# Kernel optimization log

Measured on AMD Instinct MI355X. Metric: run time of the kernel, lower is better.

The kernel has to match this reference:

```python
import jax, jax.numpy as jnp
import numpy as np

N_NODES = 50000
N_EDGES = 800000
N_GRAPHS = 64
F_IN = 256
F_HID = 256
F_OUT = 128


def setup_inputs() -> dict:
    key = jax.random.key(0)
    ks = jax.random.split(key, 8)
    x = jax.random.normal(ks[0], (N_NODES, F_IN), jnp.float32)
    edge_index = jax.random.randint(ks[1], (2, N_EDGES), 0, N_NODES, jnp.int32)
    batch = jnp.sort(jax.random.randint(ks[2], (N_NODES,), 0, N_GRAPHS, jnp.int32))
    W1 = jax.random.normal(ks[3], (F_IN, F_HID), jnp.float32) / np.sqrt(F_IN)
    b1 = jnp.zeros((F_HID,), jnp.float32)
    W2 = jax.random.normal(ks[4], (F_HID, F_HID), jnp.float32) / np.sqrt(F_HID)
    b2 = jnp.zeros((F_HID,), jnp.float32)
    Wfc = jax.random.normal(ks[5], (3 * F_HID, F_OUT), jnp.float32) / np.sqrt(3 * F_HID)
    bfc = jnp.zeros((F_OUT,), jnp.float32)
    return {"x": x, "edge_index": edge_index, "batch": batch, "n_graphs": N_GRAPHS,
            "W1": W1, "b1": b1, "W2": W2, "b2": b2, "Wfc": Wfc, "bfc": bfc}


def _gcn_layer(h, src, dst, norm, W, b, n_nodes):
    # transform first (F_in -> F_out), then gather-normalize-scatter
    h = h @ W                                      # [N, F]
    msg = h[src] * norm[:, None]                   # [E+N, F]
    agg = jax.ops.segment_sum(msg, dst, num_segments=n_nodes)
    return agg + b


def reference(x, edge_index, batch, n_graphs, W1, b1, W2, b2, Wfc, bfc):
    n = x.shape[0]
    # eval mode: dropout_adj / F.dropout are identity
    loops = jnp.arange(n, dtype=edge_index.dtype)
    src = jnp.concatenate([edge_index[0], loops])  # A + I
    dst = jnp.concatenate([edge_index[1], loops])
    # symmetric normalization D^-1/2 (A+I) D^-1/2 (degree counted at dst)
    deg = jax.ops.segment_sum(jnp.ones_like(dst, jnp.float32), dst, num_segments=n)
    dinv = jax.lax.rsqrt(jnp.maximum(deg, 1.0))    # deg >= 1 (self loops)
    norm = dinv[src] * dinv[dst]

    h = jax.nn.relu(_gcn_layer(x, src, dst, norm, W1, b1, n))
    h = jax.nn.relu(_gcn_layer(h, src, dst, norm, W2, b2, n))

    # triple global pooling over graph ids
    sums = jax.ops.segment_sum(h, batch, num_segments=n_graphs)           # add pool
    cnts = jax.ops.segment_sum(jnp.ones((n,), h.dtype), batch, num_segments=n_graphs)
    mean = sums / jnp.maximum(cnts, 1.0)[:, None]                          # mean pool
    mx = jax.ops.segment_max(h, batch, num_segments=n_graphs)             # max pool
    mx = jnp.where(jnp.isfinite(mx), mx, 0.0)                              # empty-segment guard

    g = jnp.concatenate([mean, mx, sums], axis=1)  # [G, 3*F_HID]
    return g @ Wfc + bfc
```

## Files before the change

kernel.cpp:

```cpp
#include <hip/hip_runtime.h>

#define N_NODES 50000
#define N_EDGES 800000
#define N_GRAPHS 64
#define F 256
#define F_OUT 128
#define G_DIM 768
#define SCAN_NB ((N_NODES + 255) / 256)
#define POOL_CHUNKS 32

typedef unsigned short ushort_t;
typedef short short8 __attribute__((ext_vector_type(8)));
typedef unsigned short ushort8 __attribute__((ext_vector_type(8)));
typedef unsigned short ushort4v __attribute__((ext_vector_type(4)));
typedef float float4v __attribute__((ext_vector_type(4)));
typedef float f32x2 __attribute__((ext_vector_type(2)));
typedef unsigned int uint4v __attribute__((ext_vector_type(4)));

__device__ __forceinline__ unsigned short f2bf(float f) {
    unsigned int u = __float_as_uint(f);
    u += 0x7FFFu + ((u >> 16) & 1u);
    return (unsigned short)(u >> 16);
}
__device__ __forceinline__ float bf2f(unsigned short s) {
    return __uint_as_float(((unsigned int)s) << 16);
}

__device__ __forceinline__ unsigned char fp8_enc(float v) {
#if __has_builtin(__builtin_amdgcn_cvt_pk_fp8_f32)
    return (unsigned char)__builtin_amdgcn_cvt_pk_fp8_f32(v, v, 0, false);
#else
    float x = v * 0x1p-120f;
    unsigned int u = __float_as_uint(x);
    unsigned int mag = u & 0x7FFFFFFFu;
    unsigned int r = mag + 0x0007FFFFu + ((mag >> 20) & 1u);
    unsigned int em = r >> 20;
    if (em > 0x7Eu) em = 0x7Eu;
    return (unsigned char)(em | ((u >> 24) & 0x80u));
#endif
}

__device__ __forceinline__ void fp8x4_dec(unsigned int u, float* o) {
#if __has_builtin(__builtin_amdgcn_cvt_pk_f32_fp8)
    f32x2 d0 = __builtin_amdgcn_cvt_pk_f32_fp8((int)u, false);
    f32x2 d1 = __builtin_amdgcn_cvt_pk_f32_fp8((int)u, true);
    o[0] = d0[0]; o[1] = d0[1]; o[2] = d1[0]; o[3] = d1[1];
#else
#pragma unroll
    for (int i = 0; i < 4; ++i) {
        unsigned int b = (u >> (8 * i)) & 0xFFu;
        unsigned int bits = ((b & 0x7Fu) << 20) | ((b & 0x80u) << 24);
        o[i] = __uint_as_float(bits) * 0x1p+120f;
    }
#endif
}

__device__ __forceinline__ void gld_lds16(const void* gsrc, void* ldst) {
    __builtin_amdgcn_global_load_lds(
        (const __attribute__((address_space(1))) unsigned int*)gsrc,
        (__attribute__((address_space(3))) unsigned int*)ldst, 16, 0, 0);
}

__global__ void prep_w_deg(const float* __restrict__ W1, const float* __restrict__ W2,
                           short* __restrict__ hi1, short* __restrict__ lo1,
                           short* __restrict__ hi2, short* __restrict__ lo2,
                           const int* __restrict__ dst, int* __restrict__ deg) {
    int blk = blockIdx.x;
    if (blk < 512) {
        const float* W = (blk < 256) ? W1 : W2;
        short* hi = (blk < 256) ? hi1 : hi2;
        short* lo = (blk < 256) ? lo1 : lo2;
        int n = blk & 255;
        int k = threadIdx.x;
        float v = W[k * 256 + n];
        unsigned short h = f2bf(v);
        hi[n * 256 + k] = (short)h;
        lo[n * 256 + k] = (short)f2bf(v - bf2f(h));
    } else {
        int e = (blk - 512) * 256 + threadIdx.x;
        if (e < N_EDGES) atomicAdd(&deg[dst[e]], 1);
    }
}

__global__ void scan_blocks(const int* __restrict__ deg, int* __restrict__ row_ptr,
                            int* __restrict__ block_tot, float* __restrict__ dinv) {
    __shared__ int sd[256];
    int t = threadIdx.x;
    int idx = blockIdx.x * 256 + t;
    int v = (idx < N_NODES) ? deg[idx] : 0;
    if (idx < N_NODES) dinv[idx] = rsqrtf((float)(v + 1));
    sd[t] = v;
    __syncthreads();
    for (int off = 1; off < 256; off <<= 1) {
        int a = (t >= off) ? sd[t - off] : 0;
        __syncthreads();
        sd[t] += a;
        __syncthreads();
    }
    if (idx < N_NODES) row_ptr[idx] = sd[t] - v;
    if (t == 255) block_tot[blockIdx.x] = sd[255];
}

__global__ void add_offsets(int* __restrict__ row_ptr, const int* __restrict__ block_tot) {
    __shared__ int sd[256];
    int t = threadIdx.x;
    int blk = blockIdx.x;
    sd[t] = (t < blk && t < SCAN_NB) ? block_tot[t] : 0;
    __syncthreads();
    for (int off = 128; off > 0; off >>= 1) {
        if (t < off) sd[t] += sd[t + off];
        __syncthreads();
    }
    int base = sd[0];
    int idx = blk * 256 + t;
    if (idx < N_NODES) row_ptr[idx] += base;
    if (idx == 0) row_ptr[N_NODES] = N_EDGES;
}

__global__ void bucket_edges(const int* __restrict__ src, const int* __restrict__ dst,
                             const float* __restrict__ dinv,
                             const int* __restrict__ row_ptr, int* __restrict__ cursor,
                             unsigned int* __restrict__ erec) {
    int e = blockIdx.x * blockDim.x + threadIdx.x;
    if (e < N_EDGES) {
        int d = dst[e];
        int s = src[e];
        int pos = row_ptr[d] + atomicAdd(&cursor[d], 1);
        unsigned int w = (unsigned int)f2bf(dinv[s] * dinv[d]);
        erec[pos] = (unsigned int)s | (w << 16);
    }
}

#define BM 64
#define BK 32
__global__ __launch_bounds__(256) void gemm_mfma(
        const float* __restrict__ A,
        const short* __restrict__ Bthi, const short* __restrict__ Btlo,
        unsigned char* __restrict__ h8, int M) {
    __shared__ short sAh[BM * BK], sAl[BM * BK];
    __shared__ short sBh[256 * BK], sBl[256 * BK];
    int tid = threadIdx.x;
    int wave = tid >> 6, lane = tid & 63;
    int q = lane >> 4, t = lane & 15;
    int row0 = blockIdx.x * BM;
    int wc = wave * 64;

    int lrow = lane >> 2;
    int lk = (lane & 3) * 8;
    int ar = tid >> 2;
    int ak = (tid & 3) * 8;

    int ga = row0 + ar; if (ga >= M) ga = M - 1;
    const float* abase = &A[(size_t)ga * 256 + ak];
    float4 a0 = *(const float4*)(abase);
    float4 a1 = *(const float4*)(abase + 4);

    float4v acc[4][4] = {};
    for (int kt = 0; kt < 256; kt += BK) {
#pragma unroll
        for (int j = 0; j < 4; ++j) {
            int n = wave * 64 + j * 16 + lrow;
            size_t boff = (size_t)n * 256 + kt + lk;
            int ldso = wave * 2048 + j * 512 + lane * 8;
            gld_lds16(&Bthi[boff], &sBh[ldso]);
            gld_lds16(&Btlo[boff], &sBl[ldso]);
        }
        {
            short8 h, l;
            unsigned short hh;
            hh = f2bf(a0.x); h[0] = (short)hh; l[0] = (short)f2bf(a0.x - bf2f(hh));
            hh = f2bf(a0.y); h[1] = (short)hh; l[1] = (short)f2bf(a0.y - bf2f(hh));
            hh = f2bf(a0.z); h[2] = (short)hh; l[2] = (short)f2bf(a0.z - bf2f(hh));
            hh = f2bf(a0.w); h[3] = (short)hh; l[3] = (short)f2bf(a0.w - bf2f(hh));
            hh = f2bf(a1.x); h[4] = (short)hh; l[4] = (short)f2bf(a1.x - bf2f(hh));
            hh = f2bf(a1.y); h[5] = (short)hh; l[5] = (short)f2bf(a1.y - bf2f(hh));
            hh = f2bf(a1.z); h[6] = (short)hh; l[6] = (short)f2bf(a1.z - bf2f(hh));
            hh = f2bf(a1.w); h[7] = (short)hh; l[7] = (short)f2bf(a1.w - bf2f(hh));
            *(short8*)&sAh[ar * BK + ak] = h;
            *(short8*)&sAl[ar * BK + ak] = l;
        }
        float4 na0 = a0, na1 = a1;
        if (kt + BK < 256) {
            na0 = *(const float4*)(abase + kt + BK);
            na1 = *(const float4*)(abase + kt + BK + 4);
        }
        __syncthreads();
        short8 ah[4], al[4], bh[4], bl[4];
#pragma unroll
        for (int mi = 0; mi < 4; ++mi) {
            int r = mi * 16 + t;
            ah[mi] = *(const short8*)&sAh[r * BK + q * 8];
            al[mi] = *(const short8*)&sAl[r * BK + q * 8];
        }
#pragma unroll
        for (int ni = 0; ni < 4; ++ni) {
            int n = wc + ni * 16 + t;
            bh[ni] = *(const short8*)&sBh[n * BK + q * 8];
            bl[ni] = *(const short8*)&sBl[n * BK + q * 8];
        }
#pragma unroll
        for (int mi = 0; mi < 4; ++mi)
#pragma unroll
            for (int ni = 0; ni < 4; ++ni) {
                acc[mi][ni] = __builtin_amdgcn_mfma_f32_16x16x32_bf16(ah[mi], bh[ni], acc[mi][ni], 0, 0, 0);
                acc[mi][ni] = __builtin_amdgcn_mfma_f32_16x16x32_bf16(ah[mi], bl[ni], acc[mi][ni], 0, 0, 0);
                acc[mi][ni] = __builtin_amdgcn_mfma_f32_16x16x32_bf16(al[mi], bh[ni], acc[mi][ni], 0, 0, 0);
            }
        __syncthreads();
        a0 = na0; a1 = na1;
    }
#pragma unroll
    for (int mi = 0; mi < 4; ++mi) {
        int gr0 = row0 + mi * 16 + q * 4;
#pragma unroll
        for (int rr = 0; rr < 4; ++rr) {
            int gr = gr0 + rr;
            if (gr < M) {
#pragma unroll
                for (int ni = 0; ni < 4; ++ni)
                    h8[(size_t)gr * 256 + wc + ni * 16 + t] = fp8_enc(acc[mi][ni][rr]);
            }
        }
    }
}

__global__ __launch_bounds__(256) void gemm_mfma_bf16(
        const ushort_t* __restrict__ A,
        const short* __restrict__ Bthi, const short* __restrict__ Btlo,
        unsigned char* __restrict__ h8, int M) {
    __shared__ short sA[BM * BK];
    __shared__ short sBh[256 * BK], sBl[256 * BK];
    int tid = threadIdx.x;
    int wave = tid >> 6, lane = tid & 63;
    int q = lane >> 4, t = lane & 15;
    int row0 = blockIdx.x * BM;
    int wc = wave * 64;

    int lrow = lane >> 2;
    int lk = (lane & 3) * 8;
    int ar = tid >> 2;
    int ak = (tid & 3) * 8;

    int ga = row0 + ar; if (ga >= M) ga = M - 1;
    const ushort_t* abase = &A[(size_t)ga * 256 + ak];
    ushort8 areg[8];
#pragma unroll
    for (int i = 0; i < 8; ++i) areg[i] = *(const ushort8*)(abase + i * BK);

    float4v acc[4][4] = {};
#pragma unroll
    for (int ki = 0; ki < 8; ++ki) {
        int kt = ki * BK;
#pragma unroll
        for (int j = 0; j < 4; ++j) {
            int n = wave * 64 + j * 16 + lrow;
            size_t boff = (size_t)n * 256 + kt + lk;
            int ldso = wave * 2048 + j * 512 + lane * 8;
            gld_lds16(&Bthi[boff], &sBh[ldso]);
            gld_lds16(&Btlo[boff], &sBl[ldso]);
        }
        *(ushort8*)&sA[ar * BK + ak] = areg[ki];
        __syncthreads();
        short8 ah[4], bh[4], bl[4];
#pragma unroll
        for (int mi = 0; mi < 4; ++mi) {
            int r = mi * 16 + t;
            ah[mi] = *(const short8*)&sA[r * BK + q * 8];
        }
#pragma unroll
        for (int ni = 0; ni < 4; ++ni) {
            int n = wc + ni * 16 + t;
            bh[ni] = *(const short8*)&sBh[n * BK + q * 8];
            bl[ni] = *(const short8*)&sBl[n * BK + q * 8];
        }
#pragma unroll
        for (int mi = 0; mi < 4; ++mi)
#pragma unroll
            for (int ni = 0; ni < 4; ++ni) {
                acc[mi][ni] = __builtin_amdgcn_mfma_f32_16x16x32_bf16(ah[mi], bh[ni], acc[mi][ni], 0, 0, 0);
                acc[mi][ni] = __builtin_amdgcn_mfma_f32_16x16x32_bf16(ah[mi], bl[ni], acc[mi][ni], 0, 0, 0);
            }
        __syncthreads();
    }
#pragma unroll
    for (int mi = 0; mi < 4; ++mi) {
        int gr0 = row0 + mi * 16 + q * 4;
#pragma unroll
        for (int rr = 0; rr < 4; ++rr) {
            int gr = gr0 + rr;
            if (gr < M) {
#pragma unroll
                for (int ni = 0; ni < 4; ++ni)
                    h8[(size_t)gr * 256 + wc + ni * 16 + t] = fp8_enc(acc[mi][ni][rr]);
            }
        }
    }
}

__global__ __launch_bounds__(256) void gather_fp8(
        const int* __restrict__ row_ptr, const unsigned int* __restrict__ erec,
        const float* __restrict__ dinv,
        const unsigned char* __restrict__ h8, const float* __restrict__ b,
        ushort_t* __restrict__ outBf) {
    int wave = threadIdx.x >> 6;
    int node = blockIdx.x * 4 + wave;
    int lane = threadIdx.x & 63;
    int g = lane >> 4;
    int hl = lane & 15;
    int beg = row_ptr[node], end = row_ptr[node + 1];
    float dd = dinv[node];
    float acc[16] = {};
    for (int cbeg = beg; cbeg < end; cbeg += 64) {
        int n = end - cbeg; if (n > 64) n = 64;
        unsigned int ev = 0u;
        if (lane < n) ev = __builtin_nontemporal_load(&erec[cbeg + lane]);
        int niter = (n + 15) & ~15;
        for (int k = 0; k < niter; k += 16) {
            unsigned int er0 = (unsigned int)__shfl((int)ev, k + g);
            unsigned int er1 = (unsigned int)__shfl((int)ev, k + 4 + g);
            unsigned int er2 = (unsigned int)__shfl((int)ev, k + 8 + g);
            unsigned int er3 = (unsigned int)__shfl((int)ev, k + 12 + g);
            uint4v p0 = *(const uint4v*)&h8[(size_t)((er0 & 0xFFFFu) * 256u + (unsigned)hl * 16u)];
            uint4v p1 = *(const uint4v*)&h8[(size_t)((er1 & 0xFFFFu) * 256u + (unsigned)hl * 16u)];
            uint4v p2 = *(const uint4v*)&h8[(size_t)((er2 & 0xFFFFu) * 256u + (unsigned)hl * 16u)];
            uint4v p3 = *(const uint4v*)&h8[(size_t)((er3 & 0xFFFFu) * 256u + (unsigned)hl * 16u)];
            float w0 = bf2f((unsigned short)(er0 >> 16));
            float w1 = bf2f((unsigned short)(er1 >> 16));
            float w2 = bf2f((unsigned short)(er2 >> 16));
            float w3 = bf2f((unsigned short)(er3 >> 16));
            float d0[4], d1[4], d2[4], d3[4];
#pragma unroll
            for (int wdi = 0; wdi < 4; ++wdi) {
                fp8x4_dec(p0[wdi], d0);
                fp8x4_dec(p1[wdi], d1);
                fp8x4_dec(p2[wdi], d2);
                fp8x4_dec(p3[wdi], d3);
#pragma unroll
                for (int j = 0; j < 4; ++j) {
                    int a = wdi * 4 + j;
                    acc[a] = fmaf(d0[j], w0, acc[a]);
                    acc[a] = fmaf(d1[j], w1, acc[a]);
                    acc[a] = fmaf(d2[j], w2, acc[a]);
                    acc[a] = fmaf(d3[j], w3, acc[a]);
                }
            }
        }
    }
#pragma unroll
    for (int j = 0; j < 16; ++j) {
        acc[j] += __shfl_xor(acc[j], 16);
        acc[j] += __shfl_xor(acc[j], 32);
    }
    if (g == 0) {
        uint4v sp = *(const uint4v*)&h8[(size_t)node * 256 + hl * 16];
        float sf[16];
        fp8x4_dec(sp[0], &sf[0]);
        fp8x4_dec(sp[1], &sf[4]);
        fp8x4_dec(sp[2], &sf[8]);
        fp8x4_dec(sp[3], &sf[12]);
        float4 b0 = *(const float4*)&b[hl * 16];
        float4 b1 = *(const float4*)&b[hl * 16 + 4];
        float4 b2 = *(const float4*)&b[hl * 16 + 8];
        float4 b3 = *(const float4*)&b[hl * 16 + 12];
        float bb[16] = {b0.x, b0.y, b0.z, b0.w, b1.x, b1.y, b1.z, b1.w,
                        b2.x, b2.y, b2.z, b2.w, b3.x, b3.y, b3.z, b3.w};
        float ws = dd * dd;
        ushort8 o0, o1;
#pragma unroll
        for (int j = 0; j < 8; ++j) {
            float v0 = fmaxf(fmaf(sf[j], ws, acc[j]) + bb[j], 0.f);
            o0[j] = f2bf(v0);
            float v1 = fmaxf(fmaf(sf[8 + j], ws, acc[8 + j]) + bb[8 + j], 0.f);
            o1[j] = f2bf(v1);
        }
        __builtin_nontemporal_store(o0, (ushort8*)&outBf[(size_t)node * 256 + hl * 16]);
        __builtin_nontemporal_store(o1, (ushort8*)&outBf[(size_t)node * 256 + hl * 16 + 8]);
    }
}

__global__ __launch_bounds__(64) void pool_partial(
        const ushort_t* __restrict__ h, const int* __restrict__ batch,
        float* __restrict__ psum, int* __restrict__ pmaxi) {
    int g = blockIdx.x;
    int chunk = blockIdx.y;
    int lane = threadIdx.x;
    int lo = 0, hi = N_NODES;
    while (lo < hi) { int mid = (lo + hi) >> 1; if (batch[mid] < g) lo = mid + 1; else hi = mid; }
    int start = lo;
    lo = 0; hi = N_NODES;
    while (lo < hi) { int mid = (lo + hi) >> 1; if (batch[mid] < g + 1) lo = mid + 1; else hi = mid; }
    int end = lo;
    int len = end - start;
    if (len <= 0) return;
    int per = (len + POOL_CHUNKS - 1) / POOL_CHUNKS;
    int cs = start + chunk * per;
    int ce = cs + per; if (ce > end) ce = end;
    if (cs >= ce) return;
    float4 sum = make_float4(0.f, 0.f, 0.f, 0.f);
    float4 mx  = make_float4(0.f, 0.f, 0.f, 0.f);
    for (int n = cs; n < ce; ++n) {
        ushort4v u = *(const ushort4v*)&h[(size_t)n * 256 + lane * 4];
        float vx = bf2f(u.x), vy = bf2f(u.y), vz = bf2f(u.z), vw = bf2f(u.w);
        sum.x += vx; sum.y += vy; sum.z += vz; sum.w += vw;
        mx.x = fmaxf(mx.x, vx); mx.y = fmaxf(mx.y, vy);
        mx.z = fmaxf(mx.z, vz); mx.w = fmaxf(mx.w, vw);
    }
    float* ps = &psum[g * F + lane * 4];
    atomicAdd(&ps[0], sum.x); atomicAdd(&ps[1], sum.y);
    atomicAdd(&ps[2], sum.z); atomicAdd(&ps[3], sum.w);
    int* pm = &pmaxi[g * F + lane * 4];
    atomicMax(&pm[0], __float_as_int(mx.x)); atomicMax(&pm[1], __float_as_int(mx.y));
    atomicMax(&pm[2], __float_as_int(mx.z)); atomicMax(&pm[3], __float_as_int(mx.w));
}

__global__ void final_gemm(const float* __restrict__ psum, const int* __restrict__ pmaxi,
                           const int* __restrict__ batch,
                           const float* __restrict__ Wfc, const float* __restrict__ bfc,
                           float* __restrict__ out) {
    int g = blockIdx.x;
    int o = threadIdx.x;
    __shared__ float row[G_DIM];
    __shared__ int s_cnt;
    if (threadIdx.x == 0) {
        int lo = 0, hi = N_NODES;
        while (lo < hi) { int mid = (lo + hi) >> 1; if (batch[mid] < g) lo = mid + 1; else hi = mid; }
        int start = lo;
        lo = 0; hi = N_NODES;
        while (lo < hi) { int mid = (lo + hi) >> 1; if (batch[mid] < g + 1) lo = mid + 1; else hi = mid; }
        s_cnt = lo - start;
    }
    __syncthreads();
    float inv = 1.0f / fmaxf((float)s_cnt, 1.0f);
    for (int i = threadIdx.x; i < F; i += 128) {
        float s = psum[g * F + i];
        row[i]       = s * inv;
        row[F + i]   = __int_as_float(pmaxi[g * F + i]);
        row[2*F + i] = s;
    }
    __syncthreads();
    float acc = bfc[o];
    for (int k = 0; k < G_DIM; ++k) acc += row[k] * Wfc[k * F_OUT + o];
    out[g * F_OUT + o] = acc;
}

extern "C" void kernel_launch(void* const* d_in, const int* in_sizes, int n_in,
                              void* d_out, int out_size, void* d_ws, size_t ws_size,
                              hipStream_t stream) {
    const float* x    = (const float*)d_in[0];
    const int*   ei   = (const int*)d_in[1];
    const int*   batch= (const int*)d_in[2];
    const float* W1   = (const float*)d_in[4];
    const float* b1   = (const float*)d_in[5];
    const float* W2   = (const float*)d_in[6];
    const float* b2   = (const float*)d_in[7];
    const float* Wfc  = (const float*)d_in[8];
    const float* bfc  = (const float*)d_in[9];
    float* out = (float*)d_out;

    const int* src = ei;
    const int* dst = ei + N_EDGES;

    const size_t NF = (size_t)N_NODES * F;

    unsigned char* h8 = (unsigned char*)d_ws;
    ushort_t* h1bf = (ushort_t*)(h8 + NF);
    ushort_t* h2bf = h1bf;
    short* w1hi  = (short*)(h1bf + NF);
    short* w1lo  = w1hi + 65536;
    short* w2hi  = w1lo + 65536;
    short* w2lo  = w2hi + 65536;
    float* dinv  = (float*)(w2lo + 65536);
    int*   deg   = (int*)(dinv + N_NODES);
    int*   cursor= deg + N_NODES;
    float* psum  = (float*)(cursor + N_NODES);
    int*   pmaxi = (int*)(psum + N_GRAPHS * F);
    int*   row_ptr = pmaxi + N_GRAPHS * F;
    int*   btot  = row_ptr + N_NODES + 1;
    unsigned int* erec = (unsigned int*)(btot + 256);

    hipMemsetAsync(deg, 0, (2 * N_NODES + 2 * N_GRAPHS * F) * sizeof(int), stream);
    prep_w_deg<<<512 + (N_EDGES + 255) / 256, 256, 0, stream>>>(
        W1, W2, w1hi, w1lo, w2hi, w2lo, dst, deg);
    scan_blocks<<<SCAN_NB, 256, 0, stream>>>(deg, row_ptr, btot, dinv);
    add_offsets<<<SCAN_NB, 256, 0, stream>>>(row_ptr, btot);
    bucket_edges<<<(N_EDGES + 255) / 256, 256, 0, stream>>>(src, dst, dinv, row_ptr,
                                                            cursor, erec);

    int ggemm = (N_NODES + BM - 1) / BM;
    int ngb = N_NODES / 4;

    gemm_mfma<<<ggemm, 256, 0, stream>>>(x, w1hi, w1lo, h8, N_NODES);
    gather_fp8<<<ngb, 256, 0, stream>>>(row_ptr, erec, dinv, h8, b1, h1bf);

    gemm_mfma_bf16<<<ggemm, 256, 0, stream>>>(h1bf, w2hi, w2lo, h8, N_NODES);
    gather_fp8<<<ngb, 256, 0, stream>>>(row_ptr, erec, dinv, h8, b2, h2bf);

    pool_partial<<<dim3(N_GRAPHS, POOL_CHUNKS), 64, 0, stream>>>(h2bf, batch, psum, pmaxi);
    final_gemm<<<N_GRAPHS, F_OUT, 0, stream>>>(psum, pmaxi, batch, Wfc, bfc, out);
}
```

Measured before the change: 356.1 us.

## Fuse edge bucketing into first GEMM launch and drop A-lo split term

Merges the edge-bucketing kernel into the first GEMM launch: extra blocks past the GEMM grid do the CSR bucketing while the GEMM blocks run, removing one launch and letting the two independent jobs overlap. It also drops the low-order bf16 split of the fp32 input x, going from three MFMA products per tile to two and removing the sAl shared buffer. That cuts MFMA work and LDS traffic but lowers GEMM precision on x, although the output is stored as fp8 anyway.

```diff
diff --git a/kernel.cpp b/kernel.cpp
--- a/kernel.cpp
+++ b/kernel.cpp
@@ -8,6 +8,7 @@
 #define G_DIM 768
 #define SCAN_NB ((N_NODES + 255) / 256)
 #define POOL_CHUNKS 32
+#define EBLK ((N_EDGES + 255) / 256)
 
 typedef unsigned short ushort_t;
 typedef short short8 __attribute__((ext_vector_type(8)));
@@ -117,28 +118,30 @@
     if (idx == 0) row_ptr[N_NODES] = N_EDGES;
 }
 
-__global__ void bucket_edges(const int* __restrict__ src, const int* __restrict__ dst,
-                             const float* __restrict__ dinv,
-                             const int* __restrict__ row_ptr, int* __restrict__ cursor,
-                             unsigned int* __restrict__ erec) {
-    int e = blockIdx.x * blockDim.x + threadIdx.x;
-    if (e < N_EDGES) {
-        int d = dst[e];
-        int s = src[e];
-        int pos = row_ptr[d] + atomicAdd(&cursor[d], 1);
-        unsigned int w = (unsigned int)f2bf(dinv[s] * dinv[d]);
-        erec[pos] = (unsigned int)s | (w << 16);
-    }
-}
-
 #define BM 64
 #define BK 32
-__global__ __launch_bounds__(256) void gemm_mfma(
+__global__ __launch_bounds__(256) void gemm1_bucket(
         const float* __restrict__ A,
         const short* __restrict__ Bthi, const short* __restrict__ Btlo,
-        unsigned char* __restrict__ h8, int M) {
-    __shared__ short sAh[BM * BK], sAl[BM * BK];
+        unsigned char* __restrict__ h8, int M,
+        const int* __restrict__ src, const int* __restrict__ dst,
+        const float* __restrict__ dinv, const int* __restrict__ row_ptr,
+        int* __restrict__ cursor, unsigned int* __restrict__ erec, int ngemm) {
+    __shared__ short sAh[BM * BK];
     __shared__ short sBh[256 * BK], sBl[256 * BK];
+
+    if (blockIdx.x >= ngemm) {
+        int e = (blockIdx.x - ngemm) * 256 + threadIdx.x;
+        if (e < N_EDGES) {
+            int d = dst[e];
+            int s = src[e];
+            int pos = row_ptr[d] + atomicAdd(&cursor[d], 1);
+            unsigned int w = (unsigned int)f2bf(dinv[s] * dinv[d]);
+            erec[pos] = (unsigned int)s | (w << 16);
+        }
+        return;
+    }
+
     int tid = threadIdx.x;
     int wave = tid >> 6, lane = tid & 63;
     int q = lane >> 4, t = lane & 15;
@@ -166,18 +169,12 @@
             gld_lds16(&Btlo[boff], &sBl[ldso]);
         }
         {
-            short8 h, l;
-            unsigned short hh;
-            hh = f2bf(a0.x); h[0] = (short)hh; l[0] = (short)f2bf(a0.x - bf2f(hh));
-            hh = f2bf(a0.y); h[1] = (short)hh; l[1] = (short)f2bf(a0.y - bf2f(hh));
-            hh = f2bf(a0.z); h[2] = (short)hh; l[2] = (short)f2bf(a0.z - bf2f(hh));
-            hh = f2bf(a0.w); h[3] = (short)hh; l[3] = (short)f2bf(a0.w - bf2f(hh));
-            hh = f2bf(a1.x); h[4] = (short)hh; l[4] = (short)f2bf(a1.x - bf2f(hh));
-            hh = f2bf(a1.y); h[5] = (short)hh; l[5] = (short)f2bf(a1.y - bf2f(hh));
-            hh = f2bf(a1.z); h[6] = (short)hh; l[6] = (short)f2bf(a1.z - bf2f(hh));
-            hh = f2bf(a1.w); h[7] = (short)hh; l[7] = (short)f2bf(a1.w - bf2f(hh));
+            short8 h;
+            h[0] = (short)f2bf(a0.x); h[1] = (short)f2bf(a0.y);
+            h[2] = (short)f2bf(a0.z); h[3] = (short)f2bf(a0.w);
+            h[4] = (short)f2bf(a1.x); h[5] = (short)f2bf(a1.y);
+            h[6] = (short)f2bf(a1.z); h[7] = (short)f2bf(a1.w);
             *(short8*)&sAh[ar * BK + ak] = h;
-            *(short8*)&sAl[ar * BK + ak] = l;
         }
         float4 na0 = a0, na1 = a1;
         if (kt + BK < 256) {
@@ -185,12 +182,11 @@
             na1 = *(const float4*)(abase + kt + BK + 4);
         }
         __syncthreads();
-        short8 ah[4], al[4], bh[4], bl[4];
+        short8 ah[4], bh[4], bl[4];
 #pragma unroll
         for (int mi = 0; mi < 4; ++mi) {
             int r = mi * 16 + t;
             ah[mi] = *(const short8*)&sAh[r * BK + q * 8];
-            al[mi] = *(const short8*)&sAl[r * BK + q * 8];
         }
 #pragma unroll
         for (int ni = 0; ni < 4; ++ni) {
@@ -204,7 +200,6 @@
             for (int ni = 0; ni < 4; ++ni) {
                 acc[mi][ni] = __builtin_amdgcn_mfma_f32_16x16x32_bf16(ah[mi], bh[ni], acc[mi][ni], 0, 0, 0);
                 acc[mi][ni] = __builtin_amdgcn_mfma_f32_16x16x32_bf16(ah[mi], bl[ni], acc[mi][ni], 0, 0, 0);
-                acc[mi][ni] = __builtin_amdgcn_mfma_f32_16x16x32_bf16(al[mi], bh[ni], acc[mi][ni], 0, 0, 0);
             }
         __syncthreads();
         a0 = na0; a1 = na1;
@@ -483,13 +478,12 @@
         W1, W2, w1hi, w1lo, w2hi, w2lo, dst, deg);
     scan_blocks<<<SCAN_NB, 256, 0, stream>>>(deg, row_ptr, btot, dinv);
     add_offsets<<<SCAN_NB, 256, 0, stream>>>(row_ptr, btot);
-    bucket_edges<<<(N_EDGES + 255) / 256, 256, 0, stream>>>(src, dst, dinv, row_ptr,
-                                                            cursor, erec);
 
     int ggemm = (N_NODES + BM - 1) / BM;
     int ngb = N_NODES / 4;
 
-    gemm_mfma<<<ggemm, 256, 0, stream>>>(x, w1hi, w1lo, h8, N_NODES);
+    gemm1_bucket<<<ggemm + EBLK, 256, 0, stream>>>(
+        x, w1hi, w1lo, h8, N_NODES, src, dst, dinv, row_ptr, cursor, erec, ggemm);
     gather_fp8<<<ngb, 256, 0, stream>>>(row_ptr, erec, dinv, h8, b1, h1bf);
 
     gemm_mfma_bf16<<<ggemm, 256, 0, stream>>>(h1bf, w2hi, w2lo, h8, N_NODES);
```

After: 350.1 us. No clear change (-1.7%).
